# Performance work log

Hardware: AMD Instinct MI355X
Metric: run time of the kernel (lower is better)

The kernel has to match this reference:

```python
import jax, jax.numpy as jnp
import numpy as np

B, S, HID = 16, 1024, 768
NH, HD = 12, 64  # num_heads, head_dim


def setup_inputs() -> dict:
    key = jax.random.key(0)
    ks = jax.random.split(key, 10)
    s = 0.02
    return {
        "hidden_states": jax.random.normal(ks[0], (B, S, HID), jnp.float32),
        "channel_importance": jnp.ones((HID,), jnp.float32),
        "context_importance": jnp.ones((HID,), jnp.float32),
        # Linear weights stored as (in, out): y = x @ W + b (== torch x @ W_t.T + b)
        "Wq": jax.random.normal(ks[1], (HID, HID), jnp.float32) * s,
        "bq": jnp.zeros((HID,), jnp.float32),
        "Wk": jax.random.normal(ks[2], (HID, HID), jnp.float32) * s,
        "bk": jnp.zeros((HID,), jnp.float32),
        "Wv": jax.random.normal(ks[3], (HID, HID), jnp.float32) * s,
        "bv": jnp.zeros((HID,), jnp.float32),
        "Wo": jax.random.normal(ks[4], (HID, HID), jnp.float32) * s,
        "bo": jnp.zeros((HID,), jnp.float32),
    }


def reference(hidden_states, channel_importance, context_importance,
              Wq, bq, Wk, bk, Wv, bv, Wo, bo):
    # channel-importance scaling (prune=False branch skipped)
    h = hidden_states * channel_importance  # [B,S,HID]
    # Q/K/V projections, split into heads: [B,S,HID] -> [B,NH,S,HD]
    def heads(x):
        return x.reshape(B, S, NH, HD).transpose(0, 2, 1, 3)
    q = heads(h @ Wq + bq)
    k = heads(h @ Wk + bk)
    v = heads(h @ Wv + bv)
    # scaled dot-product attention (dropout rate 0 -> identity)
    scores = jnp.einsum('bhqd,bhkd->bhqk', q, k) / jnp.sqrt(jnp.float32(HD))
    probs = jax.nn.softmax(scores, axis=-1)
    ctx = jnp.einsum('bhqk,bhkd->bhqd', probs, v)
    ctx = ctx.transpose(0, 2, 1, 3).reshape(B, S, HID)
    # context channel-importance scaling, then output projection
    ctx = ctx * context_importance
    out = ctx @ Wo + bo
    return out  # weights=None since visualize=False
```

## Files before the change

kernel.cpp:

```cpp
#include <hip/hip_runtime.h>
#include <hip/hip_bf16.h>

typedef unsigned short u16;
typedef short bf16x8 __attribute__((ext_vector_type(8)));
typedef float f32x4 __attribute__((ext_vector_type(4)));
typedef float f32x16 __attribute__((ext_vector_type(16)));
typedef unsigned short u16x4 __attribute__((ext_vector_type(4)));
typedef unsigned u32x4 __attribute__((ext_vector_type(4)));

#define SCALE_Q 0.18033688011112042f

__device__ __forceinline__ u16 f2b(float f) {
    __hip_bfloat16 h = __float2bfloat16(f);
    return *reinterpret_cast<u16*>(&h);
}

__device__ __forceinline__ unsigned cvt_pk_bf16(float lo, float hi) {
    unsigned r;
    asm("v_cvt_pk_bf16_f32 %0, %1, %2" : "=v"(r) : "v"(lo), "v"(hi));
    return r;
}

#define hw_exp2 __builtin_amdgcn_exp2f
#define hw_rcp  __builtin_amdgcn_rcpf

__device__ __forceinline__ void load_lds16(const void* g, void* l) {
    __builtin_amdgcn_global_load_lds(
        (const __attribute__((address_space(1))) void*)g,
        (__attribute__((address_space(3))) void*)l, 16, 0, 0);
}

__global__ __launch_bounds__(256) void prep_hidden(
    const float* __restrict__ x, const float* __restrict__ ci, u16* __restrict__ hbuf) {
    size_t i = ((size_t)blockIdx.x * 256 + threadIdx.x) * 4;
    float4 v = *(const float4*)(x + i);
    int c = (int)(i % 768);
    u16x4 o;
    o.x = f2b(v.x * ci[c]);     o.y = f2b(v.y * ci[c + 1]);
    o.z = f2b(v.z * ci[c + 2]); o.w = f2b(v.w * ci[c + 3]);
    *(u16x4*)(hbuf + i) = o;
}

__global__ __launch_bounds__(256) void transpose_w(
    const float* __restrict__ Wq, const float* __restrict__ Wk,
    const float* __restrict__ Wv, const float* __restrict__ Wo,
    const float* __restrict__ cc, u16* __restrict__ wqkvt, u16* __restrict__ wot) {
    __shared__ float tile[32][33];
    int z = blockIdx.z;
    const float* src = (z == 0) ? Wq : (z == 1) ? Wk : (z == 2) ? Wv : Wo;
    u16* dst = (z < 3) ? (wqkvt + (size_t)z * 768 * 768) : wot;
    int tx = threadIdx.x & 31, ty = threadIdx.x >> 5;
    int k0 = blockIdx.x * 32, n0 = blockIdx.y * 32;
    #pragma unroll
    for (int i = ty; i < 32; i += 8) {
        float v = src[(size_t)(k0 + i) * 768 + n0 + tx];
        if (z == 3) v *= cc[k0 + i];
        if (z == 0) v *= SCALE_Q;
        tile[i][tx] = v;
    }
    __syncthreads();
    #pragma unroll
    for (int i = ty; i < 32; i += 8)
        dst[(size_t)(n0 + i) * 768 + k0 + tx] = f2b(tile[tx][i]);
}

__global__ __launch_bounds__(256) void bias_cat(
    const float* __restrict__ bq, const float* __restrict__ bk,
    const float* __restrict__ bv, float* __restrict__ biasq) {
    int i = blockIdx.x * 256 + threadIdx.x;
    biasq[i] = (i < 768) ? bq[i] * SCALE_Q : (i < 1536) ? bk[i - 768] : bv[i - 1536];
}

template <int F32OUT>
__global__ __launch_bounds__(256) void gemm_bt(
    const u16* __restrict__ A, const u16* __restrict__ Bt,
    const float* __restrict__ bias, void* __restrict__ Cout,
    int M, int N, int K, int NTN) {
    __shared__ u16 lA[128 * 64];
    __shared__ u16 lB[128 * 64];
    int nwg = gridDim.x;
    int bid = blockIdx.x;
    int wg = ((nwg & 7) == 0) ? ((bid & 7) * (nwg >> 3) + (bid >> 3)) : bid;
    int mt = wg / NTN, nt = wg % NTN;
    int row0 = mt << 7, col0 = nt << 7;
    int tid = threadIdx.x;
    int lane = tid & 63, wv = tid >> 6;
    int wm = (wv >> 1) * 64, wn = (wv & 1) * 64;
    int l15 = lane & 15, hi = lane >> 4;

    f32x4 acc[4][4] = {};

    for (int kt = 0; kt < K; kt += 64) {
        __syncthreads();
        #pragma unroll
        for (int p = 0; p < 4; ++p) {
            int cl = p * 256 + tid;
            int rr = cl >> 3;
            int cc = (cl & 7) ^ (rr & 7);
            int lo = (p * 256 + (wv << 6)) << 3;
            load_lds16(A + (size_t)(row0 + rr) * K + kt + cc * 8, &lA[lo]);
            load_lds16(Bt + (size_t)(col0 + rr) * K + kt + cc * 8, &lB[lo]);
        }
        __syncthreads();
        __builtin_amdgcn_s_setprio(1);
        #pragma unroll
        for (int ks = 0; ks < 2; ++ks) {
            bf16x8 af[4], bf[4];
            #pragma unroll
            for (int i = 0; i < 4; ++i) {
                int ra = wm + i * 16 + l15;
                af[i] = *(const bf16x8*)&lA[ra * 64 + (((ks << 2) + hi) ^ (ra & 7)) * 8];
                int rb = wn + i * 16 + l15;
                bf[i] = *(const bf16x8*)&lB[rb * 64 + (((ks << 2) + hi) ^ (rb & 7)) * 8];
            }
            #pragma unroll
            for (int mi = 0; mi < 4; ++mi)
                #pragma unroll
                for (int ni = 0; ni < 4; ++ni)
                    acc[mi][ni] = __builtin_amdgcn_mfma_f32_16x16x32_bf16(
                        af[mi], bf[ni], acc[mi][ni], 0, 0, 0);
        }
        __builtin_amdgcn_s_setprio(0);
    }

    #pragma unroll
    for (int mi = 0; mi < 4; ++mi) {
        int rbase = row0 + wm + mi * 16 + hi * 4;
        #pragma unroll
        for (int ni = 0; ni < 4; ++ni) {
            int c = col0 + wn + ni * 16 + l15;
            float bv = bias[c];
            #pragma unroll
            for (int j = 0; j < 4; ++j) {
                float o = acc[mi][ni][j] + bv;
                if (F32OUT) ((float*)Cout)[(size_t)(rbase + j) * N + c] = o;
                else        ((u16*)Cout)[(size_t)(rbase + j) * N + c] = f2b(o);
            }
        }
    }
}

__global__ __launch_bounds__(256, 3) void attn_kernel(
    const u16* __restrict__ QKV, u16* __restrict__ ctx) {
    __shared__ u16 lK[2][64 * 64];
    __shared__ u16 lV[2][64 * 68];

    int bid = blockIdx.x;
    int wg = (bid & 7) * 192 + (bid >> 3);
    int bh = wg >> 3, qt = wg & 7;
    int b = bh / 12, h = bh % 12;
    int tid = threadIdx.x;
    int lane = tid & 63, wv = tid >> 6;
    int l31 = lane & 31;
    int hb = lane >> 5;

    const u16* Qb = QKV + (size_t)b * 1024 * 2304 + h * 64;
    const u16* Kb = Qb + 768;
    const u16* Vb = Qb + 1536;

    int qrow0 = qt * 128 + wv * 32;

    bf16x8 qf[4];
    #pragma unroll
    for (int ks = 0; ks < 4; ++ks)
        qf[ks] = *(const bf16x8*)(Qb + (size_t)(qrow0 + l31) * 2304 + ks * 16 + hb * 8);

    bf16x8 ones;
    #pragma unroll
    for (int i = 0; i < 8; ++i) ones[i] = (short)0x3F80;

    f32x16 accO0 = {}, accO1 = {};
    f32x16 accL = {};

    int jj0 = (tid & 31) * 2;
    int jjs = (jj0 & ~12) | ((jj0 & 4) << 1) | ((jj0 & 8) >> 1);
    int d0v = (tid >> 5) << 3;

    #pragma unroll
    for (int p = 0; p < 2; ++p) {
        int rr = (p * 256 + tid) >> 3;
        int cc = ((p * 256 + tid) & 7) ^ (rr & 7);
        load_lds16(Kb + (size_t)rr * 2304 + cc * 8, &lK[0][(p * 256 + (wv << 6)) << 3]);
    }
    {
        bf16x8 g0 = *(const bf16x8*)(Vb + (size_t)jj0 * 2304 + d0v);
        bf16x8 g1 = *(const bf16x8*)(Vb + (size_t)(jj0 + 1) * 2304 + d0v);
        const unsigned* a0 = (const unsigned*)&g0;
        const unsigned* a1 = (const unsigned*)&g1;
        #pragma unroll
        for (int w = 0; w < 4; ++w) {
            *(unsigned*)&lV[0][(d0v + 2 * w) * 68 + jjs] =
                __builtin_amdgcn_perm(a1[w], a0[w], 0x05040100);
            *(unsigned*)&lV[0][(d0v + 2 * w + 1) * 68 + jjs] =
                __builtin_amdgcn_perm(a1[w], a0[w], 0x07060302);
        }
    }
    __syncthreads();

    int cur = 0;
    for (int t = 0; t < 16; ++t) {
        bf16x8 nv0, nv1;
        if (t < 15) {
            size_t kt1 = (size_t)(t + 1) * 64;
            #pragma unroll
            for (int p = 0; p < 2; ++p) {
                int rr = (p * 256 + tid) >> 3;
                int cc = ((p * 256 + tid) & 7) ^ (rr & 7);
                load_lds16(Kb + (kt1 + rr) * 2304 + cc * 8,
                           &lK[cur ^ 1][(p * 256 + (wv << 6)) << 3]);
            }
            nv0 = *(const bf16x8*)(Vb + (kt1 + jj0) * 2304 + d0v);
            nv1 = *(const bf16x8*)(Vb + (kt1 + jj0 + 1) * 2304 + d0v);
        }

        #pragma unroll
        for (int kvb = 0; kvb < 2; ++kvb) {
            f32x16 accs = {};
            __builtin_amdgcn_s_setprio(1);
            #pragma unroll
            for (int ks = 0; ks < 4; ++ks) {
                bf16x8 kf = *(const bf16x8*)&lK[cur][
                    (kvb * 32 + l31) * 64 + (((ks << 1) + hb) ^ (l31 & 7)) * 8];
                accs = __builtin_amdgcn_mfma_f32_32x32x16_bf16(kf, qf[ks], accs, 0, 0, 0);
            }
            __builtin_amdgcn_s_setprio(0);

            unsigned W[8];
            #pragma unroll
            for (int w = 0; w < 8; ++w)
                W[w] = cvt_pk_bf16(hw_exp2(accs[2 * w]), hw_exp2(accs[2 * w + 1]));

            __builtin_amdgcn_s_setprio(1);
            #pragma unroll
            for (int mm = 0; mm < 2; ++mm) {
                int m = kvb * 2 + mm;
                u32x4 pw;
                pw.x = W[4 * mm];     pw.y = W[4 * mm + 1];
                pw.z = W[4 * mm + 2]; pw.w = W[4 * mm + 3];
                bf16x8 pa = *(bf16x8*)&pw;
                accL = __builtin_amdgcn_mfma_f32_32x32x16_bf16(pa, ones, accL, 0, 0, 0);
                bf16x8 vf0 = *(const bf16x8*)&lV[cur][l31 * 68 + m * 16 + hb * 8];
                bf16x8 vf1 = *(const bf16x8*)&lV[cur][(32 + l31) * 68 + m * 16 + hb * 8];
                accO0 = __builtin_amdgcn_mfma_f32_32x32x16_bf16(pa, vf0, accO0, 0, 0, 0);
                accO1 = __builtin_amdgcn_mfma_f32_32x32x16_bf16(pa, vf1, accO1, 0, 0, 0);
            }
            __builtin_amdgcn_s_setprio(0);
        }

        if (t < 15) {
            const unsigned* a0 = (const unsigned*)&nv0;
            const unsigned* a1 = (const unsigned*)&nv1;
            #pragma unroll
            for (int w = 0; w < 4; ++w) {
                *(unsigned*)&lV[cur ^ 1][(d0v + 2 * w) * 68 + jjs] =
                    __builtin_amdgcn_perm(a1[w], a0[w], 0x05040100);
                *(unsigned*)&lV[cur ^ 1][(d0v + 2 * w + 1) * 68 + jjs] =
                    __builtin_amdgcn_perm(a1[w], a0[w], 0x07060302);
            }
        }

        __syncthreads();
        cur ^= 1;
    }

    #pragma unroll
    for (int r = 0; r < 16; ++r) {
        float inv = hw_rcp(accL[r]);
        int q = (r & 3) + 8 * (r >> 2) + hb * 4;
        size_t row = (size_t)(b * 1024 + qrow0 + q);
        ctx[row * 768 + h * 64 + l31]      = f2b(accO0[r] * inv);
        ctx[row * 768 + h * 64 + 32 + l31] = f2b(accO1[r] * inv);
    }
}

extern "C" void kernel_launch(void* const* d_in, const int* in_sizes, int n_in,
                              void* d_out, int out_size, void* d_ws, size_t ws_size,
                              hipStream_t stream) {
    const float* x  = (const float*)d_in[0];
    const float* ci = (const float*)d_in[1];
    const float* cc = (const float*)d_in[2];
    const float* Wq = (const float*)d_in[3];
    const float* bq = (const float*)d_in[4];
    const float* Wk = (const float*)d_in[5];
    const float* bk = (const float*)d_in[6];
    const float* Wv = (const float*)d_in[7];
    const float* bv = (const float*)d_in[8];
    const float* Wo = (const float*)d_in[9];
    const float* bo = (const float*)d_in[10];
    float* out = (float*)d_out;

    unsigned char* ws = (unsigned char*)d_ws;
    size_t off = 0;
    auto alloc = [&](size_t bytes) {
        void* p = ws + off;
        off += (bytes + 255) & ~(size_t)255;
        return p;
    };
    u16*   hbuf  = (u16*)  alloc((size_t)16384 * 768 * 2);
    u16*   wqkvt = (u16*)  alloc((size_t)2304 * 768 * 2);
    u16*   wot   = (u16*)  alloc((size_t)768 * 768 * 2);
    float* biasq = (float*)alloc(2304 * 4);
    u16*   qkv   = (u16*)  alloc((size_t)16384 * 2304 * 2);
    u16*   ctx   = (u16*)  alloc((size_t)16384 * 768 * 2);

    prep_hidden<<<12288, 256, 0, stream>>>(x, ci, hbuf);
    transpose_w<<<dim3(24, 24, 4), 256, 0, stream>>>(Wq, Wk, Wv, Wo, cc, wqkvt, wot);
    bias_cat<<<9, 256, 0, stream>>>(bq, bk, bv, biasq);
    gemm_bt<0><<<2304, 256, 0, stream>>>(hbuf, wqkvt, biasq, qkv, 16384, 2304, 768, 18);
    attn_kernel<<<1536, 256, 0, stream>>>(qkv, ctx);
    gemm_bt<1><<<768, 256, 0, stream>>>(ctx, wot, bo, out, 16384, 768, 768, 6);
}
```

Measured before the change: 185.5 us.

## Halve attention KV tile and replace ones-MFMA row sum with scalar accumulation

The attention kernel now processes 32-key tiles instead of 64, halving LDS per block and raising the launch-bounds occupancy target from 3 to 6 blocks per CU. The softmax denominator is no longer computed by an extra MFMA against a ones matrix. Each lane sums its exponentials in a scalar, and the sums are combined with cross-lane shuffles at the end. This removes a quarter of the MFMAs and a 16-register accumulator, but doubles the number of loop iterations and barriers. It also shifts the row-sum to fp32 VALU adds on unrounded values, so it no longer sums the bf16-rounded probabilities.

```diff
diff --git a/kernel.cpp b/kernel.cpp
--- a/kernel.cpp
+++ b/kernel.cpp
@@ -140,10 +140,10 @@
     }
 }
 
-__global__ __launch_bounds__(256, 3) void attn_kernel(
+__global__ __launch_bounds__(256, 6) void attn_kernel(
     const u16* __restrict__ QKV, u16* __restrict__ ctx) {
-    __shared__ u16 lK[2][64 * 64];
-    __shared__ u16 lV[2][64 * 68];
+    __shared__ u16 lK[2][32 * 64];
+    __shared__ u16 lV[2][64 * 34];
 
     int bid = blockIdx.x;
     int wg = (bid & 7) * 192 + (bid >> 3);
@@ -165,96 +165,87 @@
     for (int ks = 0; ks < 4; ++ks)
         qf[ks] = *(const bf16x8*)(Qb + (size_t)(qrow0 + l31) * 2304 + ks * 16 + hb * 8);
 
-    bf16x8 ones;
-    #pragma unroll
-    for (int i = 0; i < 8; ++i) ones[i] = (short)0x3F80;
-
     f32x16 accO0 = {}, accO1 = {};
-    f32x16 accL = {};
-
-    int jj0 = (tid & 31) * 2;
+    float lacc = 0.f;
+
+    int krr = tid >> 3;
+    int kcc = (tid & 7) ^ (krr & 7);
+    bool vstage = tid < 128;
+    int jj0 = (tid & 15) * 2;
     int jjs = (jj0 & ~12) | ((jj0 & 4) << 1) | ((jj0 & 8) >> 1);
-    int d0v = (tid >> 5) << 3;
-
-    #pragma unroll
-    for (int p = 0; p < 2; ++p) {
-        int rr = (p * 256 + tid) >> 3;
-        int cc = ((p * 256 + tid) & 7) ^ (rr & 7);
-        load_lds16(Kb + (size_t)rr * 2304 + cc * 8, &lK[0][(p * 256 + (wv << 6)) << 3]);
-    }
-    {
+    int d0v = ((tid >> 4) & 7) << 3;
+
+    load_lds16(Kb + (size_t)krr * 2304 + kcc * 8, &lK[0][(wv << 6) << 3]);
+    if (vstage) {
         bf16x8 g0 = *(const bf16x8*)(Vb + (size_t)jj0 * 2304 + d0v);
         bf16x8 g1 = *(const bf16x8*)(Vb + (size_t)(jj0 + 1) * 2304 + d0v);
         const unsigned* a0 = (const unsigned*)&g0;
         const unsigned* a1 = (const unsigned*)&g1;
         #pragma unroll
         for (int w = 0; w < 4; ++w) {
-            *(unsigned*)&lV[0][(d0v + 2 * w) * 68 + jjs] =
+            *(unsigned*)&lV[0][(d0v + 2 * w) * 34 + jjs] =
                 __builtin_amdgcn_perm(a1[w], a0[w], 0x05040100);
-            *(unsigned*)&lV[0][(d0v + 2 * w + 1) * 68 + jjs] =
+            *(unsigned*)&lV[0][(d0v + 2 * w + 1) * 34 + jjs] =
                 __builtin_amdgcn_perm(a1[w], a0[w], 0x07060302);
         }
     }
     __syncthreads();
 
     int cur = 0;
-    for (int t = 0; t < 16; ++t) {
+    for (int t = 0; t < 32; ++t) {
         bf16x8 nv0, nv1;
-        if (t < 15) {
-            size_t kt1 = (size_t)(t + 1) * 64;
-            #pragma unroll
-            for (int p = 0; p < 2; ++p) {
-                int rr = (p * 256 + tid) >> 3;
-                int cc = ((p * 256 + tid) & 7) ^ (rr & 7);
-                load_lds16(Kb + (kt1 + rr) * 2304 + cc * 8,
-                           &lK[cur ^ 1][(p * 256 + (wv << 6)) << 3]);
+        if (t < 31) {
+            size_t kt1 = (size_t)(t + 1) * 32;
+            load_lds16(Kb + (kt1 + krr) * 2304 + kcc * 8, &lK[cur ^ 1][(wv << 6) << 3]);
+            if (vstage) {
+                nv0 = *(const bf16x8*)(Vb + (kt1 + jj0) * 2304 + d0v);
+                nv1 = *(const bf16x8*)(Vb + (kt1 + jj0 + 1) * 2304 + d0v);
             }
-            nv0 = *(const bf16x8*)(Vb + (kt1 + jj0) * 2304 + d0v);
-            nv1 = *(const bf16x8*)(Vb + (kt1 + jj0 + 1) * 2304 + d0v);
-        }
-
-        #pragma unroll
-        for (int kvb = 0; kvb < 2; ++kvb) {
-            f32x16 accs = {};
-            __builtin_amdgcn_s_setprio(1);
-            #pragma unroll
-            for (int ks = 0; ks < 4; ++ks) {
-                bf16x8 kf = *(const bf16x8*)&lK[cur][
-                    (kvb * 32 + l31) * 64 + (((ks << 1) + hb) ^ (l31 & 7)) * 8];
-                accs = __builtin_amdgcn_mfma_f32_32x32x16_bf16(kf, qf[ks], accs, 0, 0, 0);
-            }
-            __builtin_amdgcn_s_setprio(0);
-
-            unsigned W[8];
-            #pragma unroll
-            for (int w = 0; w < 8; ++w)
-                W[w] = cvt_pk_bf16(hw_exp2(accs[2 * w]), hw_exp2(accs[2 * w + 1]));
-
-            __builtin_amdgcn_s_setprio(1);
-            #pragma unroll
-            for (int mm = 0; mm < 2; ++mm) {
-                int m = kvb * 2 + mm;
-                u32x4 pw;
-                pw.x = W[4 * mm];     pw.y = W[4 * mm + 1];
-                pw.z = W[4 * mm + 2]; pw.w = W[4 * mm + 3];
-                bf16x8 pa = *(bf16x8*)&pw;
-                accL = __builtin_amdgcn_mfma_f32_32x32x16_bf16(pa, ones, accL, 0, 0, 0);
-                bf16x8 vf0 = *(const bf16x8*)&lV[cur][l31 * 68 + m * 16 + hb * 8];
-                bf16x8 vf1 = *(const bf16x8*)&lV[cur][(32 + l31) * 68 + m * 16 + hb * 8];
-                accO0 = __builtin_amdgcn_mfma_f32_32x32x16_bf16(pa, vf0, accO0, 0, 0, 0);
-                accO1 = __builtin_amdgcn_mfma_f32_32x32x16_bf16(pa, vf1, accO1, 0, 0, 0);
-            }
-            __builtin_amdgcn_s_setprio(0);
-        }
-
-        if (t < 15) {
+        }
+
+        f32x16 accs = {};
+        __builtin_amdgcn_s_setprio(1);
+        #pragma unroll
+        for (int ks = 0; ks < 4; ++ks) {
+            bf16x8 kf = *(const bf16x8*)&lK[cur][
+                l31 * 64 + (((ks << 1) + hb) ^ (l31 & 7)) * 8];
+            accs = __builtin_amdgcn_mfma_f32_32x32x16_bf16(kf, qf[ks], accs, 0, 0, 0);
+        }
+        __builtin_amdgcn_s_setprio(0);
+
+        unsigned W[8];
+        float ls = 0.f;
+        #pragma unroll
+        for (int w = 0; w < 8; ++w) {
+            float e0 = hw_exp2(accs[2 * w]);
+            float e1 = hw_exp2(accs[2 * w + 1]);
+            ls += e0 + e1;
+            W[w] = cvt_pk_bf16(e0, e1);
+        }
+        lacc += ls;
+
+        __builtin_amdgcn_s_setprio(1);
+        #pragma unroll
+        for (int mm = 0; mm < 2; ++mm) {
+            u32x4 pw;
+            pw.x = W[4 * mm];     pw.y = W[4 * mm + 1];
+            pw.z = W[4 * mm + 2]; pw.w = W[4 * mm + 3];
+            bf16x8 pa = *(bf16x8*)&pw;
+            bf16x8 vf0 = *(const bf16x8*)&lV[cur][l31 * 34 + mm * 16 + hb * 8];
+            bf16x8 vf1 = *(const bf16x8*)&lV[cur][(32 + l31) * 34 + mm * 16 + hb * 8];
+            accO0 = __builtin_amdgcn_mfma_f32_32x32x16_bf16(pa, vf0, accO0, 0, 0, 0);
+            accO1 = __builtin_amdgcn_mfma_f32_32x32x16_bf16(pa, vf1, accO1, 0, 0, 0);
+        }
+        __builtin_amdgcn_s_setprio(0);
+
+        if (t < 31 && vstage) {
             const unsigned* a0 = (const unsigned*)&nv0;
             const unsigned* a1 = (const unsigned*)&nv1;
             #pragma unroll
             for (int w = 0; w < 4; ++w) {
-                *(unsigned*)&lV[cur ^ 1][(d0v + 2 * w) * 68 + jjs] =
+                *(unsigned*)&lV[cur ^ 1][(d0v + 2 * w) * 34 + jjs] =
                     __builtin_amdgcn_perm(a1[w], a0[w], 0x05040100);
-                *(unsigned*)&lV[cur ^ 1][(d0v + 2 * w + 1) * 68 + jjs] =
+                *(unsigned*)&lV[cur ^ 1][(d0v + 2 * w + 1) * 34 + jjs] =
                     __builtin_amdgcn_perm(a1[w], a0[w], 0x07060302);
             }
         }
@@ -263,10 +254,12 @@
         cur ^= 1;
     }
 
+    float lsum = lacc + __shfl_xor(lacc, 32);
     #pragma unroll
     for (int r = 0; r < 16; ++r) {
-        float inv = hw_rcp(accL[r]);
         int q = (r & 3) + 8 * (r >> 2) + hb * 4;
+        float Lr = __shfl(lsum, q);
+        float inv = hw_rcp(Lr);
         size_t row = (size_t)(b * 1024 + qrow0 + q);
         ctx[row * 768 + h * 64 + l31]      = f2b(accO0[r] * inv);
         ctx[row * 768 + h * 64 + 32 + l31] = f2b(accO1[r] * inv);
```

Measured after the change: 275.6 us. 48.5% more time.
